# Kernel tuning notes

Measured on AMD Instinct MI355X. Metric: run time of the kernel, lower is better.

Reference implementation:

```python
import jax, jax.numpy as jnp
import numpy as np

B, S, IN, OUT, L = 8, 2048, 4096, 64, 16

def setup_inputs() -> dict:
    key = jax.random.key(0)
    k1, k2, k3 = jax.random.split(key, 3)
    x = jax.random.normal(k1, (B, S, IN), dtype=jnp.float32)
    adapter_ids = jax.random.randint(k2, (B,), 0, L)
    weight = jax.random.normal(k3, (L, OUT, IN), dtype=jnp.float32) * 0.02
    return {"x": x, "adapter_ids": adapter_ids, "weight": weight}

def reference(x, adapter_ids, weight):
    # Gather one [OUT, IN] weight per batch element, then per-sample linear.
    # Equivalent to the torch loop: stack_i F.linear(x[i], weight[adapter_ids[i]]).
    w = weight[adapter_ids]                      # [B, OUT, IN]
    return jnp.einsum('bsi,boi->bso', x, w)      # [B, S, OUT]
```

## Files before the change

### kernel.cpp

```cpp
#include <hip/hip_runtime.h>
#include <hip/hip_bf16.h>
#include <stdint.h>

#define NB   8
#define NS   2048
#define NIN  4096
#define NOUT 64
#define NL   16

typedef __attribute__((ext_vector_type(8))) short s16x8;
typedef __attribute__((ext_vector_type(4))) float f32x4;

__device__ __forceinline__ unsigned short f2bf(float f) {
    union { float f; unsigned u; } v; v.f = f;
    unsigned u = v.u + 0x7fffu + ((v.u >> 16) & 1u);
    return (unsigned short)(u >> 16);
}

__device__ __forceinline__ s16x8 pack8(float4 a, float4 b) {
    s16x8 r;
    r[0] = (short)f2bf(a.x); r[1] = (short)f2bf(a.y);
    r[2] = (short)f2bf(a.z); r[3] = (short)f2bf(a.w);
    r[4] = (short)f2bf(b.x); r[5] = (short)f2bf(b.y);
    r[6] = (short)f2bf(b.z); r[7] = (short)f2bf(b.w);
    return r;
}

__global__ __launch_bounds__(256) void convert_w_kernel(const float* __restrict__ w,
                                                        unsigned short* __restrict__ o) {
    size_t i = ((size_t)blockIdx.x * 256 + threadIdx.x) * 8;
    const float4* src = (const float4*)(w + i);
    float4 a = src[0], b = src[1];
    *(s16x8*)(o + i) = pack8(a, b);
}

constexpr int MT  = 32;
constexpr int KT  = 64;
constexpr int NKT = NIN / KT;

template <bool WBF16>
__global__ __launch_bounds__(256) void mll_kernel(const float* __restrict__ x,
                                                  const int* __restrict__ ids,
                                                  const void* __restrict__ wsel,
                                                  float* __restrict__ out) {
    __shared__ __align__(16) unsigned short xs[2 * MT * KT];

    const int bx   = blockIdx.x;
    const int b    = bx >> 6;
    const int mt   = bx & 63;
    const int aid  = ids[b];
    const int t    = threadIdx.x;
    const int lane = t & 63;
    const int wv   = t >> 6;

    const float* xbase = x + ((size_t)b * NS + (size_t)mt * MT) * NIN;

    const int srow   = t >> 3;
    const int schunk = t & 7;
    const float* gsrc = xbase + (size_t)srow * NIN + schunk * 8;
    const int soff = srow * KT + ((schunk ^ (srow & 7)) * 8);

    const int l15 = lane & 15;
    const int lk  = lane >> 4;

    const unsigned short* wb16 = nullptr;
    const float*          wb32 = nullptr;
    if (WBF16) wb16 = (const unsigned short*)wsel + ((size_t)aid * NOUT + wv * 16 + l15) * NIN + lk * 8;
    else       wb32 = (const float*)wsel          + ((size_t)aid * NOUT + wv * 16 + l15) * NIN + lk * 8;

    f32x4 acc0 = {0.f, 0.f, 0.f, 0.f};
    f32x4 acc1 = {0.f, 0.f, 0.f, 0.f};

    {
        const float4* g0 = (const float4*)gsrc;
        float4 c0 = g0[0], c1 = g0[1];
        *(s16x8*)(xs + soff) = pack8(c0, c1);
    }
    const float4* g1 = (const float4*)(gsrc + KT);
    float4 r0 = g1[0], r1 = g1[1];
    __syncthreads();

    for (int tile = 0; tile < NKT; ++tile) {
        const int p = tile & 1;

        const int pt = (tile + 2 < NKT) ? (tile + 2) : (NKT - 1);
        const float4* gn = (const float4*)(gsrc + (size_t)pt * KT);
        float4 n0 = gn[0], n1 = gn[1];

        const unsigned short* buf = xs + p * (MT * KT);

#pragma unroll
        for (int s = 0; s < 2; ++s) {
            s16x8 bfrag;
            if (WBF16) {
                bfrag = *(const s16x8*)(wb16 + (size_t)tile * KT + s * 32);
            } else {
                const float4* wp = (const float4*)(wb32 + (size_t)tile * KT + s * 32);
                bfrag = pack8(wp[0], wp[1]);
            }
            const int ae = l15 * KT + (((s * 4 + lk) ^ (l15 & 7)) * 8);
            s16x8 af0 = *(const s16x8*)(buf + ae);
            s16x8 af1 = *(const s16x8*)(buf + ae + 16 * KT);
            acc0 = __builtin_amdgcn_mfma_f32_16x16x32_bf16(af0, bfrag, acc0, 0, 0, 0);
            acc1 = __builtin_amdgcn_mfma_f32_16x16x32_bf16(af1, bfrag, acc1, 0, 0, 0);
        }

        if (tile + 1 < NKT) {
            *(s16x8*)(xs + (1 - p) * (MT * KT) + soff) = pack8(r0, r1);
        }
        r0 = n0; r1 = n1;
        __syncthreads();
    }

    float* ob = out + ((size_t)b * NS + (size_t)mt * MT) * NOUT + wv * 16 + l15;
    const int rbase = lk * 4;
#pragma unroll
    for (int r = 0; r < 4; ++r) {
        ob[(size_t)(rbase + r) * NOUT]      = acc0[r];
        ob[(size_t)(16 + rbase + r) * NOUT] = acc1[r];
    }
}

extern "C" void kernel_launch(void* const* d_in, const int* in_sizes, int n_in,
                              void* d_out, int out_size, void* d_ws, size_t ws_size,
                              hipStream_t stream) {
    const float* x   = (const float*)d_in[0];
    const int*   ids = (const int*)d_in[1];
    const float* w   = (const float*)d_in[2];
    float*       out = (float*)d_out;

    const size_t wbytes = (size_t)NL * NOUT * NIN * sizeof(unsigned short);
    const int grid = NB * (NS / MT);

    if (ws_size >= wbytes) {
        unsigned short* wbf = (unsigned short*)d_ws;
        const int n = NL * NOUT * NIN;
        convert_w_kernel<<<n / (256 * 8), 256, 0, stream>>>(w, wbf);
        mll_kernel<true><<<grid, 256, 0, stream>>>(x, ids, wbf, out);
    } else {
        mll_kernel<false><<<grid, 256, 0, stream>>>(x, ids, w, out);
    }
}
```

Measured before the change: 393.4 us.

## Drop LDS staging and weight pre-conversion; load fp32 fragments directly into registers

Removes the separate weight bf16 conversion kernel and the shared-memory double buffer for x. Each wave now loads fp32 x and weight fragments straight from global memory into registers, with two tiles prefetched, and converts them with the hardware bf16 conversion builtin before the MFMA. The M tile shrinks to 16 rows so the grid doubles, and block order interleaves batches. In exchange, all four waves in a block now load the same x rows from global memory instead of sharing them through LDS. Weights are also re-read as fp32, which doubles their traffic, though that data is small and likely cached.

```diff
diff --git a/kernel.cpp b/kernel.cpp
--- a/kernel.cpp
+++ b/kernel.cpp
@@ -1,5 +1,4 @@
 #include <hip/hip_runtime.h>
-#include <hip/hip_bf16.h>
 #include <stdint.h>
 
 #define NB   8
@@ -8,116 +7,85 @@
 #define NOUT 64
 #define NL   16
 
-typedef __attribute__((ext_vector_type(8))) short s16x8;
-typedef __attribute__((ext_vector_type(4))) float f32x4;
-
-__device__ __forceinline__ unsigned short f2bf(float f) {
-    union { float f; unsigned u; } v; v.f = f;
-    unsigned u = v.u + 0x7fffu + ((v.u >> 16) & 1u);
-    return (unsigned short)(u >> 16);
-}
-
-__device__ __forceinline__ s16x8 pack8(float4 a, float4 b) {
-    s16x8 r;
-    r[0] = (short)f2bf(a.x); r[1] = (short)f2bf(a.y);
-    r[2] = (short)f2bf(a.z); r[3] = (short)f2bf(a.w);
-    r[4] = (short)f2bf(b.x); r[5] = (short)f2bf(b.y);
-    r[6] = (short)f2bf(b.z); r[7] = (short)f2bf(b.w);
-    return r;
-}
-
-__global__ __launch_bounds__(256) void convert_w_kernel(const float* __restrict__ w,
-                                                        unsigned short* __restrict__ o) {
-    size_t i = ((size_t)blockIdx.x * 256 + threadIdx.x) * 8;
-    const float4* src = (const float4*)(w + i);
-    float4 a = src[0], b = src[1];
-    *(s16x8*)(o + i) = pack8(a, b);
-}
-
-constexpr int MT  = 32;
+constexpr int MT  = 16;
 constexpr int KT  = 64;
 constexpr int NKT = NIN / KT;
 
-template <bool WBF16>
-__global__ __launch_bounds__(256) void mll_kernel(const float* __restrict__ x,
-                                                  const int* __restrict__ ids,
-                                                  const void* __restrict__ wsel,
-                                                  float* __restrict__ out) {
-    __shared__ __align__(16) unsigned short xs[2 * MT * KT];
+typedef __attribute__((ext_vector_type(8))) short  s16x8;
+typedef __attribute__((ext_vector_type(4))) float  f32x4;
+typedef __attribute__((ext_vector_type(4))) float  fv4;
+typedef __attribute__((ext_vector_type(4))) __bf16 bf16x4;
 
+__device__ __forceinline__ s16x8 cvt8(float4 a, float4 b) {
+    fv4 va = {a.x, a.y, a.z, a.w};
+    fv4 vb = {b.x, b.y, b.z, b.w};
+    union { struct { bf16x4 lo, hi; } h; s16x8 s; } u;
+    u.h.lo = __builtin_convertvector(va, bf16x4);
+    u.h.hi = __builtin_convertvector(vb, bf16x4);
+    return u.s;
+}
+
+#define LOAD_TILE(dst, base, tt)                                  \
+    {                                                             \
+        const float4* _p = (const float4*)((base) + (tt) * KT);   \
+        dst[0] = _p[0]; dst[1] = _p[1];                           \
+        dst[2] = _p[8]; dst[3] = _p[9];                           \
+    }
+
+__global__ __launch_bounds__(256, 4) void mll_kernel(const float* __restrict__ x,
+                                                     const int* __restrict__ ids,
+                                                     const float* __restrict__ w,
+                                                     float* __restrict__ out) {
     const int bx   = blockIdx.x;
-    const int b    = bx >> 6;
-    const int mt   = bx & 63;
+    const int b    = bx & 7;
+    const int mt   = bx >> 3;
     const int aid  = ids[b];
     const int t    = threadIdx.x;
     const int lane = t & 63;
     const int wv   = t >> 6;
+    const int l15  = lane & 15;
+    const int lk   = lane >> 4;
 
-    const float* xbase = x + ((size_t)b * NS + (size_t)mt * MT) * NIN;
+    const float* pa = x + ((size_t)(b * NS + mt * MT + l15)) * NIN + lk * 8;
+    const float* pb = w + ((size_t)(aid * NOUT + wv * 16 + l15)) * NIN + lk * 8;
 
-    const int srow   = t >> 3;
-    const int schunk = t & 7;
-    const float* gsrc = xbase + (size_t)srow * NIN + schunk * 8;
-    const int soff = srow * KT + ((schunk ^ (srow & 7)) * 8);
+    f32x4 acc = {0.f, 0.f, 0.f, 0.f};
 
-    const int l15 = lane & 15;
-    const int lk  = lane >> 4;
+    float4 a0[4], b0[4], a1[4], b1[4];
+    LOAD_TILE(a0, pa, 0); LOAD_TILE(b0, pb, 0);
+    LOAD_TILE(a1, pa, 1); LOAD_TILE(b1, pb, 1);
 
-    const unsigned short* wb16 = nullptr;
-    const float*          wb32 = nullptr;
-    if (WBF16) wb16 = (const unsigned short*)wsel + ((size_t)aid * NOUT + wv * 16 + l15) * NIN + lk * 8;
-    else       wb32 = (const float*)wsel          + ((size_t)aid * NOUT + wv * 16 + l15) * NIN + lk * 8;
-
-    f32x4 acc0 = {0.f, 0.f, 0.f, 0.f};
-    f32x4 acc1 = {0.f, 0.f, 0.f, 0.f};
-
+    for (int tt = 0; tt < NKT - 2; tt += 2) {
+        {
+            s16x8 af0 = cvt8(a0[0], a0[1]), bf0 = cvt8(b0[0], b0[1]);
+            s16x8 af1 = cvt8(a0[2], a0[3]), bf1 = cvt8(b0[2], b0[3]);
+            LOAD_TILE(a0, pa, tt + 2); LOAD_TILE(b0, pb, tt + 2);
+            acc = __builtin_amdgcn_mfma_f32_16x16x32_bf16(af0, bf0, acc, 0, 0, 0);
+            acc = __builtin_amdgcn_mfma_f32_16x16x32_bf16(af1, bf1, acc, 0, 0, 0);
+        }
+        {
+            s16x8 af0 = cvt8(a1[0], a1[1]), bf0 = cvt8(b1[0], b1[1]);
+            s16x8 af1 = cvt8(a1[2], a1[3]), bf1 = cvt8(b1[2], b1[3]);
+            LOAD_TILE(a1, pa, tt + 3); LOAD_TILE(b1, pb, tt + 3);
+            acc = __builtin_amdgcn_mfma_f32_16x16x32_bf16(af0, bf0, acc, 0, 0, 0);
+            acc = __builtin_amdgcn_mfma_f32_16x16x32_bf16(af1, bf1, acc, 0, 0, 0);
+        }
+    }
     {
-        const float4* g0 = (const float4*)gsrc;
-        float4 c0 = g0[0], c1 = g0[1];
-        *(s16x8*)(xs + soff) = pack8(c0, c1);
-    }
-    const float4* g1 = (const float4*)(gsrc + KT);
-    float4 r0 = g1[0], r1 = g1[1];
-    __syncthreads();
-
-    for (int tile = 0; tile < NKT; ++tile) {
-        const int p = tile & 1;
-
-        const int pt = (tile + 2 < NKT) ? (tile + 2) : (NKT - 1);
-        const float4* gn = (const float4*)(gsrc + (size_t)pt * KT);
-        float4 n0 = gn[0], n1 = gn[1];
-
-        const unsigned short* buf = xs + p * (MT * KT);
-
-#pragma unroll
-        for (int s = 0; s < 2; ++s) {
-            s16x8 bfrag;
-            if (WBF16) {
-                bfrag = *(const s16x8*)(wb16 + (size_t)tile * KT + s * 32);
-            } else {
-                const float4* wp = (const float4*)(wb32 + (size_t)tile * KT + s * 32);
-                bfrag = pack8(wp[0], wp[1]);
-            }
-            const int ae = l15 * KT + (((s * 4 + lk) ^ (l15 & 7)) * 8);
-            s16x8 af0 = *(const s16x8*)(buf + ae);
-            s16x8 af1 = *(const s16x8*)(buf + ae + 16 * KT);
-            acc0 = __builtin_amdgcn_mfma_f32_16x16x32_bf16(af0, bfrag, acc0, 0, 0, 0);
-            acc1 = __builtin_amdgcn_mfma_f32_16x16x32_bf16(af1, bfrag, acc1, 0, 0, 0);
-        }
-
-        if (tile + 1 < NKT) {
-            *(s16x8*)(xs + (1 - p) * (MT * KT) + soff) = pack8(r0, r1);
-        }
-        r0 = n0; r1 = n1;
-        __syncthreads();
+        s16x8 af0 = cvt8(a0[0], a0[1]), bf0 = cvt8(b0[0], b0[1]);
+        s16x8 af1 = cvt8(a0[2], a0[3]), bf1 = cvt8(b0[2], b0[3]);
+        acc = __builtin_amdgcn_mfma_f32_16x16x32_bf16(af0, bf0, acc, 0, 0, 0);
+        acc = __builtin_amdgcn_mfma_f32_16x16x32_bf16(af1, bf1, acc, 0, 0, 0);
+        af0 = cvt8(a1[0], a1[1]); bf0 = cvt8(b1[0], b1[1]);
+        af1 = cvt8(a1[2], a1[3]); bf1 = cvt8(b1[2], b1[3]);
+        acc = __builtin_amdgcn_mfma_f32_16x16x32_bf16(af0, bf0, acc, 0, 0, 0);
+        acc = __builtin_amdgcn_mfma_f32_16x16x32_bf16(af1, bf1, acc, 0, 0, 0);
     }
 
-    float* ob = out + ((size_t)b * NS + (size_t)mt * MT) * NOUT + wv * 16 + l15;
-    const int rbase = lk * 4;
+    float* ob = out + ((size_t)(b * NS + mt * MT)) * NOUT + wv * 16 + l15;
 #pragma unroll
     for (int r = 0; r < 4; ++r) {
-        ob[(size_t)(rbase + r) * NOUT]      = acc0[r];
-        ob[(size_t)(16 + rbase + r) * NOUT] = acc1[r];
+        ob[(size_t)(lk * 4 + r) * NOUT] = acc[r];
     }
 }
 
@@ -129,15 +97,6 @@
     const float* w   = (const float*)d_in[2];
     float*       out = (float*)d_out;
 
-    const size_t wbytes = (size_t)NL * NOUT * NIN * sizeof(unsigned short);
     const int grid = NB * (NS / MT);
-
-    if (ws_size >= wbytes) {
-        unsigned short* wbf = (unsigned short*)d_ws;
-        const int n = NL * NOUT * NIN;
-        convert_w_kernel<<<n / (256 * 8), 256, 0, stream>>>(w, wbf);
-        mll_kernel<true><<<grid, 256, 0, stream>>>(x, ids, wbf, out);
-    } else {
-        mll_kernel<false><<<grid, 256, 0, stream>>>(x, ids, w, out);
-    }
+    mll_kernel<<<grid, 256, 0, stream>>>(x, ids, w, out);
 }
```

After: 511.6 us. 1.3x slower.
